# Kernel optimization log

Hardware: AMD Instinct MI355X
Metric: run time of the kernel (lower is better)

## Reference

```python
import jax, jax.numpy as jnp
import numpy as np


def _att(h, g, adj, a1, a2):
    # h: [B,N,D], g: [B,M,D], adj: [B,N,M] (int), a1/a2: [D,1]
    e1 = jnp.matmul(h, a1)                    # [B,N,1]
    e2 = jnp.matmul(g, a2).transpose(0, 2, 1)  # [B,1,M]
    e = jax.nn.leaky_relu(e1 + e2, negative_slope=0.2)  # [B,N,M]
    neg = jnp.asarray(-9.0e15, e.dtype)
    att = jnp.where(adj > 0, e, neg)
    att = jax.nn.softmax(att, axis=2)
    att = jnp.where(jnp.isnan(att), jnp.zeros_like(att), att)
    # degree renorm: adj[bs].sum(1).repeat(M,1).T == row degree broadcast over M
    deg = jnp.sum(adj, axis=2, keepdims=True).astype(e.dtype)  # [B,N,1]
    return jnp.matmul(att * deg, g)            # [B,N,D]


def setup_inputs() -> dict:
    key = jax.random.key(0)
    ks = jax.random.split(key, 13)
    B, N1, N2 = 64, 1024, 512
    F0, F1, D = 512, 384, 256
    return {
        "x0": jax.random.normal(ks[0], (B, N1, F0), jnp.float32),
        "x1": jax.random.normal(ks[1], (B, N2, F1), jnp.float32),
        "W0": jax.random.normal(ks[2], (F0, D), jnp.float32) * (1.414 / np.sqrt(F0)),
        "W1": jax.random.normal(ks[3], (F1, D), jnp.float32) * (1.414 / np.sqrt(F1)),
        "a1_0": jax.random.normal(ks[4], (D, 1), jnp.float32) * 0.1,
        "a2_0": jax.random.normal(ks[5], (D, 1), jnp.float32) * 0.1,
        "a1_1": jax.random.normal(ks[6], (D, 1), jnp.float32) * 0.1,
        "a2_1": jax.random.normal(ks[7], (D, 1), jnp.float32) * 0.1,
        "bias": jax.random.uniform(ks[8], (D,), jnp.float32, -1.0 / np.sqrt(D), 1.0 / np.sqrt(D)),
        "adj00": jax.random.randint(ks[9], (B, N1, N1), 0, 2, jnp.int32),
        "adj01": jax.random.randint(ks[10], (B, N1, N2), 0, 2, jnp.int32),
        "adj10": jax.random.randint(ks[11], (B, N2, N1), 0, 2, jnp.int32),
        "adj11": jax.random.randint(ks[12], (B, N2, N2), 0, 2, jnp.int32),
    }


def reference(x0, x1, W0, W1, a1_0, a2_0, a1_1, a2_1, bias,
              adj00, adj01, adj10, adj11):
    h0 = jnp.matmul(x0, W0)  # [B,N1,D]
    h1 = jnp.matmul(x1, W1)  # [B,N2,D]
    o00 = _att(h0, h0, adj00, a1_0, a2_0) + bias
    o01 = _att(h0, h1, adj01, a1_0, a2_0) + bias
    o10 = _att(h1, h0, adj10, a1_1, a2_1) + bias
    o11 = _att(h1, h1, adj11, a1_1, a2_1) + bias
    return (o00, o01, o10, o11)
```

## Files before the change

kernel.cpp:

```cpp
#include <hip/hip_runtime.h>

typedef __bf16 bf16x8 __attribute__((ext_vector_type(8)));
typedef float f32x4 __attribute__((ext_vector_type(4)));

static __device__ __forceinline__ ushort f2bf(float f) {
  uint u = __builtin_bit_cast(uint, f);
  u += 0x7fffu + ((u >> 16) & 1u);
  return (ushort)(u >> 16);
}
static __device__ __forceinline__ float bf2f(ushort h) {
  uint u = ((uint)h) << 16;
  return __builtin_bit_cast(float, u);
}

__global__ void detect9(const ushort* p0, const ushort* p1, const ushort* p2,
                        const ushort* p3, const ushort* p4, const ushort* p5,
                        const ushort* p6, const ushort* p7, const ushort* p8,
                        int* flags) {
  const ushort* ps[9] = {p0, p1, p2, p3, p4, p5, p6, p7, p8};
  const ushort* p = ps[blockIdx.x];
  int t = threadIdx.x;
  ushort u = p[2 * t];
  int e = (u >> 7) & 0xFF;
  int sane = (e >= 100 && e <= 150) ? 1 : 0;
  unsigned long long m = __ballot(sane);
  if (t == 0) flags[blockIdx.x] = (__popcll(m) >= 48) ? 0 : 1;
}

static __device__ __forceinline__ float ldf(const void* p, int is32, size_t i) {
  return is32 ? ((const float*)p)[i] : bf2f(((const ushort*)p)[i]);
}

__global__ void transw(const void* W, ushort* __restrict__ WT,
                       const int* __restrict__ flags, int fi, int F) {
  int is32 = flags[fi];
  int i = blockIdx.x * 256 + threadIdx.x;
  int k = i >> 8, d = i & 255;
  ushort v = is32 ? f2bf(((const float*)W)[i]) : ((const ushort*)W)[i];
  WT[(size_t)d * F + k] = v;
}

__global__ __launch_bounds__(256) void wa_k(const void* W, const void* a1, const void* a2,
                                            const void* a3, const int* __restrict__ flags,
                                            int fW, int f1, int f2, int f3,
                                            float* __restrict__ wa, int F) {
  __shared__ float al[3][256];
  int t = threadIdx.x;
  al[0][t] = ldf(a1, flags[f1], t);
  al[1][t] = ldf(a2, flags[f2], t);
  al[2][t] = ldf(a3, flags[f3], t);
  __syncthreads();
  int k = blockIdx.x * 256 + t;
  if (k < F) {
    int w32 = flags[fW];
    float s0 = 0.f, s1 = 0.f, s2 = 0.f;
    for (int d = 0; d < 256; d++) {
      float wv = ldf(W, w32, (size_t)k * 256 + d);
      s0 += wv * al[0][d]; s1 += wv * al[1][d]; s2 += wv * al[2][d];
    }
    wa[k] = s0; wa[F + k] = s1; wa[2 * F + k] = s2;
  }
}

__global__ __launch_bounds__(256) void evec_x(const void* __restrict__ x,
                                              const float* __restrict__ wa,
                                              const int* __restrict__ flags, int fi,
                                              float* __restrict__ o1, float* __restrict__ o2,
                                              float* __restrict__ o3, int F) {
  int x32 = flags[fi];
  int node = blockIdx.x * 4 + (threadIdx.x >> 6);
  int lane = threadIdx.x & 63;
  const float* wa1 = wa, *wa2 = wa + F, *wa3 = wa + 2 * F;
  float s1 = 0.f, s2 = 0.f, s3 = 0.f;
  size_t base = (size_t)node * F;
  for (int k = lane; k < F; k += 64) {
    float xv = ldf(x, x32, base + k);
    s1 += xv * wa1[k]; s2 += xv * wa2[k]; s3 += xv * wa3[k];
  }
  #pragma unroll
  for (int off = 1; off < 64; off <<= 1) {
    s1 += __shfl_xor(s1, off); s2 += __shfl_xor(s2, off); s3 += __shfl_xor(s3, off);
  }
  if (lane == 0) { o1[node] = s1; o2[node] = s2; o3[node] = s3; }
}

__global__ __launch_bounds__(256) void gemm_h(const void* __restrict__ x,
                                              const ushort* __restrict__ WT,
                                              ushort* __restrict__ hT,
                                              const int* __restrict__ flags, int fi,
                                              int N, int F) {
  int x32 = flags[fi];
  int ntiles = N >> 6;
  int b  = blockIdx.x / ntiles;
  int n0 = (blockIdx.x % ntiles) << 6;
  __shared__ ushort Al[64][72];
  __shared__ ushort Bl[256][72];
  int t = threadIdx.x, wave = t >> 6, lane = t & 63;
  f32x4 acc[4][4] = {};

  for (int k0 = 0; k0 < F; k0 += 64) {
    #pragma unroll
    for (int i = 0; i < 2; i++) {
      int r = (t >> 3) + i * 32, g = t & 7;
      if (!x32) {
        const ushort* xb = (const ushort*)x + (size_t)(b * N + n0 + r) * F + k0;
        ((uint4*)&Al[r][0])[g] = ((const uint4*)xb)[g];
      } else {
        const float* xf = (const float*)x + (size_t)(b * N + n0 + r) * F + k0;
        float4 fa = ((const float4*)xf)[2 * g];
        float4 fb = ((const float4*)xf)[2 * g + 1];
        union { ushort u[8]; uint4 q; } pk;
        pk.u[0] = f2bf(fa.x); pk.u[1] = f2bf(fa.y); pk.u[2] = f2bf(fa.z); pk.u[3] = f2bf(fa.w);
        pk.u[4] = f2bf(fb.x); pk.u[5] = f2bf(fb.y); pk.u[6] = f2bf(fb.z); pk.u[7] = f2bf(fb.w);
        ((uint4*)&Al[r][0])[g] = pk.q;
      }
    }
    #pragma unroll
    for (int i = 0; i < 8; i++) {
      int d = (t >> 3) + i * 32, g = t & 7;
      ((uint4*)&Bl[d][0])[g] = ((const uint4*)(WT + (size_t)d * F + k0))[g];
    }
    __syncthreads();
    #pragma unroll
    for (int kh = 0; kh < 2; kh++) {
      int kk = kh * 32 + ((lane >> 4) << 3);
      bf16x8 af[4], bfr[4];
      #pragma unroll
      for (int rf = 0; rf < 4; rf++) af[rf]  = *(const bf16x8*)&Al[rf * 16 + (lane & 15)][kk];
      #pragma unroll
      for (int cf = 0; cf < 4; cf++) bfr[cf] = *(const bf16x8*)&Bl[wave * 64 + cf * 16 + (lane & 15)][kk];
      #pragma unroll
      for (int rf = 0; rf < 4; rf++)
        #pragma unroll
        for (int cf = 0; cf < 4; cf++)
          acc[rf][cf] = __builtin_amdgcn_mfma_f32_16x16x32_bf16(af[rf], bfr[cf], acc[rf][cf], 0, 0, 0);
    }
    __syncthreads();
  }
  #pragma unroll
  for (int rf = 0; rf < 4; rf++) {
    int n = n0 + rf * 16 + ((lane >> 4) << 2);
    #pragma unroll
    for (int cf = 0; cf < 4; cf++) {
      int d = wave * 64 + cf * 16 + (lane & 15);
      ushort4 v;
      v.x = f2bf(acc[rf][cf][0]); v.y = f2bf(acc[rf][cf][1]);
      v.z = f2bf(acc[rf][cf][2]); v.w = f2bf(acc[rf][cf][3]);
      *(ushort4*)(hT + ((size_t)b * 256 + d) * N + n) = v;
    }
  }
}

__global__ __launch_bounds__(256) void att(const float* __restrict__ e1,
                                           const float* __restrict__ e2,
                                           const ushort* __restrict__ gT,
                                           const int* __restrict__ adj,
                                           const void* bias,
                                           const int* __restrict__ flags,
                                           void* __restrict__ outv, size_t ooff,
                                           int Nr, int M) {
  int b32 = flags[8];
  int o32 = flags[0] | flags[1] | flags[2] | flags[3] | flags[4] |
            flags[5] | flags[6] | flags[7] | flags[8];
  int ntiles = Nr >> 6;
  int b  = blockIdx.x / ntiles;
  int n0 = (blockIdx.x % ntiles) << 6;
  __shared__ ushort Wl[64][72];
  __shared__ ushort Gl[256][72];
  __shared__ float  e2l[1024];
  __shared__ float  e1l[64];
  __shared__ float  rscale[64];
  int t = threadIdx.x, wave = t >> 6, lane = t & 63;
  for (int i = t; i < M; i += 256) e2l[i] = e2[(size_t)b * M + i];
  if (t < 64) e1l[t] = e1[(size_t)b * Nr + n0 + t];
  __syncthreads();

  f32x4 acc[4][4] = {};
  float s_part = 0.f, deg_part = 0.f;
  int r = t >> 2, mseg = (t & 3) << 4;
  float e1v = e1l[r];
  const int* adjrow = adj + ((size_t)b * Nr + n0 + r) * M;

  for (int m0 = 0; m0 < M; m0 += 64) {
    #pragma unroll
    for (int i = 0; i < 8; i++) {
      int d = (t >> 3) + i * 32, g = t & 7;
      ((uint4*)&Gl[d][0])[g] = ((const uint4*)(gT + ((size_t)b * 256 + d) * M + m0))[g];
    }
    {
      const int* ap = adjrow + m0 + mseg;
      int4 q0 = ((const int4*)ap)[0], q1 = ((const int4*)ap)[1];
      int4 q2 = ((const int4*)ap)[2], q3 = ((const int4*)ap)[3];
      int av[16] = {q0.x,q0.y,q0.z,q0.w, q1.x,q1.y,q1.z,q1.w,
                    q2.x,q2.y,q2.z,q2.w, q3.x,q3.y,q3.z,q3.w};
      union { ushort u[16]; uint4 q[2]; } pk;
      #pragma unroll
      for (int j = 0; j < 16; j++) {
        float e = e1v + e2l[m0 + mseg + j];
        e = e > 0.f ? e : 0.2f * e;
        e = fminf(e, 60.f);
        float w = (av[j] > 0) ? __expf(e) : 0.f;
        ushort wb = f2bf(w);
        s_part += bf2f(wb);
        deg_part += (float)av[j];
        pk.u[j] = wb;
      }
      *(uint4*)&Wl[r][mseg]     = pk.q[0];
      *(uint4*)&Wl[r][mseg + 8] = pk.q[1];
    }
    __syncthreads();
    #pragma unroll
    for (int kh = 0; kh < 2; kh++) {
      int kk = kh * 32 + ((lane >> 4) << 3);
      bf16x8 af[4], bfr[4];
      #pragma unroll
      for (int rf = 0; rf < 4; rf++) af[rf]  = *(const bf16x8*)&Wl[rf * 16 + (lane & 15)][kk];
      #pragma unroll
      for (int cf = 0; cf < 4; cf++) bfr[cf] = *(const bf16x8*)&Gl[wave * 64 + cf * 16 + (lane & 15)][kk];
      #pragma unroll
      for (int rf = 0; rf < 4; rf++)
        #pragma unroll
        for (int cf = 0; cf < 4; cf++)
          acc[rf][cf] = __builtin_amdgcn_mfma_f32_16x16x32_bf16(af[rf], bfr[cf], acc[rf][cf], 0, 0, 0);
    }
    __syncthreads();
  }

  s_part   += __shfl_xor(s_part, 1);   s_part   += __shfl_xor(s_part, 2);
  deg_part += __shfl_xor(deg_part, 1); deg_part += __shfl_xor(deg_part, 2);
  if ((t & 3) == 0) {
    float sc = (s_part > 0.f) ? deg_part / s_part : 0.f;
    if (!(sc > -1e38f && sc < 1e38f)) sc = 0.f;
    rscale[r] = sc;
  }
  __syncthreads();

  #pragma unroll
  for (int rf = 0; rf < 4; rf++) {
    int nbase = rf * 16 + ((lane >> 4) << 2);
    #pragma unroll
    for (int cf = 0; cf < 4; cf++) {
      int d = wave * 64 + cf * 16 + (lane & 15);
      float bi = ldf(bias, b32, d);
      #pragma unroll
      for (int j = 0; j < 4; j++) {
        int nl = nbase + j;
        float v = acc[rf][cf][j] * rscale[nl] + bi;
        size_t idx = ooff + ((size_t)(b * Nr + n0 + nl)) * 256 + d;
        if (o32) ((float*)outv)[idx] = v;
        else     ((ushort*)outv)[idx] = f2bf(v);
      }
    }
  }
}

extern "C" void kernel_launch(void* const* d_in, const int* in_sizes, int n_in,
                              void* d_out, int out_size, void* d_ws, size_t ws_size,
                              hipStream_t stream) {
  (void)in_sizes; (void)n_in; (void)out_size; (void)ws_size;
  const void* x0   = d_in[0];
  const void* x1   = d_in[1];
  const void* W0   = d_in[2];
  const void* W1   = d_in[3];
  const void* a1_0 = d_in[4];
  const void* a2_0 = d_in[5];
  const void* a1_1 = d_in[6];
  const void* a2_1 = d_in[7];
  const void* bias = d_in[8];
  const int* adj00 = (const int*)d_in[9];
  const int* adj01 = (const int*)d_in[10];
  const int* adj10 = (const int*)d_in[11];
  const int* adj11 = (const int*)d_in[12];

  const int B = 64, N1 = 1024, N2 = 512, F0 = 512, F1 = 384;
  int*    flags = (int*)d_ws;
  ushort* base = (ushort*)((char*)d_ws + 64);
  ushort* hT0 = base;
  ushort* hT1 = hT0 + (size_t)B * 256 * N1;
  ushort* WT0 = hT1 + (size_t)B * 256 * N2;
  ushort* WT1 = WT0 + (size_t)256 * F0;
  float* e1_0 = (float*)(WT1 + (size_t)256 * F1);
  float* e2a  = e1_0 + (size_t)B * N1;
  float* e2c  = e2a + (size_t)B * N1;
  float* e1_1 = e2c + (size_t)B * N1;
  float* e2b  = e1_1 + (size_t)B * N2;
  float* e2d  = e2b + (size_t)B * N2;
  float* wa0  = e2d + (size_t)B * N2;
  float* wa1  = wa0 + 3 * F0;

  detect9<<<9, 64, 0, stream>>>((const ushort*)x0, (const ushort*)x1,
                                (const ushort*)W0, (const ushort*)W1,
                                (const ushort*)a1_0, (const ushort*)a2_0,
                                (const ushort*)a1_1, (const ushort*)a2_1,
                                (const ushort*)bias, flags);

  transw<<<F0, 256, 0, stream>>>(W0, WT0, flags, 2, F0);
  transw<<<F1, 256, 0, stream>>>(W1, WT1, flags, 3, F1);
  wa_k<<<(F0 + 255) / 256, 256, 0, stream>>>(W0, a1_0, a2_0, a2_1, flags, 2, 4, 5, 7, wa0, F0);
  wa_k<<<(F1 + 255) / 256, 256, 0, stream>>>(W1, a1_1, a2_0, a2_1, flags, 3, 6, 5, 7, wa1, F1);
  gemm_h<<<B * (N1 / 64), 256, 0, stream>>>(x0, WT0, hT0, flags, 0, N1, F0);
  gemm_h<<<B * (N2 / 64), 256, 0, stream>>>(x1, WT1, hT1, flags, 1, N2, F1);
  evec_x<<<B * N1 / 4, 256, 0, stream>>>(x0, wa0, flags, 0, e1_0, e2a, e2c, F0);
  evec_x<<<B * N2 / 4, 256, 0, stream>>>(x1, wa1, flags, 1, e1_1, e2b, e2d, F1);

  const size_t o00 = 0;
  const size_t o01 = (size_t)B * N1 * 256;
  const size_t o10 = o01 + (size_t)B * N1 * 256;
  const size_t o11 = o10 + (size_t)B * N2 * 256;
  att<<<B * (N1 / 64), 256, 0, stream>>>(e1_0, e2a, hT0, adj00, bias, flags, d_out, o00, N1, N1);
  att<<<B * (N1 / 64), 256, 0, stream>>>(e1_0, e2b, hT1, adj01, bias, flags, d_out, o01, N1, N2);
  att<<<B * (N2 / 64), 256, 0, stream>>>(e1_1, e2c, hT0, adj10, bias, flags, d_out, o10, N2, N1);
  att<<<B * (N2 / 64), 256, 0, stream>>>(e1_1, e2d, hT1, adj11, bias, flags, d_out, o11, N2, N2);
}
```

Before: 1.071 ms.

## Stage B/G tiles via direct global-to-LDS loads with XOR swizzle, prefetch next tiles

Both the projection GEMM and the attention kernel now load the 256x64 weight/feature tile straight into LDS with global_load_lds, storing it unpadded with an XOR swizzle on the 16-byte chunk index. The reads apply the same swizzle to avoid bank conflicts. The x rows and adjacency values for the next k/m tile are register-prefetched one iteration ahead so their global latency overlaps the current MFMA work. This removes the VGPR round trip for the large tile and hides some load latency, at the cost of more live registers and a tighter correctness dependency on the swizzle and LDS-load layout matching.

```diff
diff --git a/kernel.cpp b/kernel.cpp
--- a/kernel.cpp
+++ b/kernel.cpp
@@ -2,6 +2,9 @@
 
 typedef __bf16 bf16x8 __attribute__((ext_vector_type(8)));
 typedef float f32x4 __attribute__((ext_vector_type(4)));
+
+#define GPTR(p) ((const __attribute__((address_space(1))) void*)(p))
+#define LPTR(p) ((__attribute__((address_space(3))) void*)(p))
 
 static __device__ __forceinline__ ushort f2bf(float f) {
   uint u = __builtin_bit_cast(uint, f);
@@ -84,6 +87,39 @@
   if (lane == 0) { o1[node] = s1; o2[node] = s2; o3[node] = s3; }
 }
 
+static __device__ __forceinline__ void stage_tile(const ushort* __restrict__ src,
+                                                  int rowstride,
+                                                  ushort* __restrict__ dst,
+                                                  int wave, int lane) {
+  int rsub = lane >> 3;
+  int gsw = ((lane & 7) ^ rsub) << 3;
+  #pragma unroll
+  for (int i = 0; i < 8; i++) {
+    int dbase = i * 32 + wave * 8;
+    __builtin_amdgcn_global_load_lds(
+        GPTR(src + (size_t)(dbase + rsub) * rowstride + gsw),
+        LPTR(dst + dbase * 64), 16, 0, 0);
+  }
+}
+
+static __device__ __forceinline__ void load_x4(uint4* dst, const void* x, int x32,
+                                               size_t rowbase, int F, int k0,
+                                               int r0, int g8) {
+  if (x32) {
+    #pragma unroll
+    for (int i = 0; i < 2; i++) {
+      const uint4* xf = (const uint4*)((const float*)x + (rowbase + (size_t)(r0 + i * 32)) * F + k0);
+      dst[2 * i] = xf[2 * g8]; dst[2 * i + 1] = xf[2 * g8 + 1];
+    }
+  } else {
+    #pragma unroll
+    for (int i = 0; i < 2; i++) {
+      const uint4* xb = (const uint4*)((const ushort*)x + (rowbase + (size_t)(r0 + i * 32)) * F + k0);
+      dst[i] = xb[g8];
+    }
+  }
+}
+
 __global__ __launch_bounds__(256) void gemm_h(const void* __restrict__ x,
                                               const ushort* __restrict__ WT,
                                               ushort* __restrict__ hT,
@@ -94,41 +130,48 @@
   int b  = blockIdx.x / ntiles;
   int n0 = (blockIdx.x % ntiles) << 6;
   __shared__ ushort Al[64][72];
-  __shared__ ushort Bl[256][72];
+  __shared__ ushort Bl[256 * 64];
   int t = threadIdx.x, wave = t >> 6, lane = t & 63;
+  int r0 = t >> 3, g8 = t & 7;
+  size_t rowbase = (size_t)(b * N + n0);
   f32x4 acc[4][4] = {};
 
-  for (int k0 = 0; k0 < F; k0 += 64) {
-    #pragma unroll
-    for (int i = 0; i < 2; i++) {
-      int r = (t >> 3) + i * 32, g = t & 7;
-      if (!x32) {
-        const ushort* xb = (const ushort*)x + (size_t)(b * N + n0 + r) * F + k0;
-        ((uint4*)&Al[r][0])[g] = ((const uint4*)xb)[g];
-      } else {
-        const float* xf = (const float*)x + (size_t)(b * N + n0 + r) * F + k0;
-        float4 fa = ((const float4*)xf)[2 * g];
-        float4 fb = ((const float4*)xf)[2 * g + 1];
+  const int nk = F >> 6;
+  uint4 xr[4], xn[4];
+  load_x4(xr, x, x32, rowbase, F, 0, r0, g8);
+
+  for (int kt = 0; kt < nk; kt++) {
+    int k0 = kt << 6;
+    int has_next = (kt + 1 < nk);
+    stage_tile(WT + k0, F, Bl, wave, lane);
+    if (has_next) load_x4(xn, x, x32, rowbase, F, k0 + 64, r0, g8);
+    if (x32) {
+      #pragma unroll
+      for (int i = 0; i < 2; i++) {
+        union { uint4 q[2]; float f[8]; } fa;
+        fa.q[0] = xr[2 * i]; fa.q[1] = xr[2 * i + 1];
         union { ushort u[8]; uint4 q; } pk;
-        pk.u[0] = f2bf(fa.x); pk.u[1] = f2bf(fa.y); pk.u[2] = f2bf(fa.z); pk.u[3] = f2bf(fa.w);
-        pk.u[4] = f2bf(fb.x); pk.u[5] = f2bf(fb.y); pk.u[6] = f2bf(fb.z); pk.u[7] = f2bf(fb.w);
-        ((uint4*)&Al[r][0])[g] = pk.q;
-      }
-    }
-    #pragma unroll
-    for (int i = 0; i < 8; i++) {
-      int d = (t >> 3) + i * 32, g = t & 7;
-      ((uint4*)&Bl[d][0])[g] = ((const uint4*)(WT + (size_t)d * F + k0))[g];
+        #pragma unroll
+        for (int j = 0; j < 8; j++) pk.u[j] = f2bf(fa.f[j]);
+        ((uint4*)&Al[r0 + i * 32][0])[g8] = pk.q;
+      }
+    } else {
+      #pragma unroll
+      for (int i = 0; i < 2; i++) ((uint4*)&Al[r0 + i * 32][0])[g8] = xr[i];
     }
     __syncthreads();
     #pragma unroll
     for (int kh = 0; kh < 2; kh++) {
       int kk = kh * 32 + ((lane >> 4) << 3);
+      int sw = (lane & 7) << 3;
       bf16x8 af[4], bfr[4];
       #pragma unroll
       for (int rf = 0; rf < 4; rf++) af[rf]  = *(const bf16x8*)&Al[rf * 16 + (lane & 15)][kk];
       #pragma unroll
-      for (int cf = 0; cf < 4; cf++) bfr[cf] = *(const bf16x8*)&Bl[wave * 64 + cf * 16 + (lane & 15)][kk];
+      for (int cf = 0; cf < 4; cf++) {
+        int d = wave * 64 + cf * 16 + (lane & 15);
+        bfr[cf] = *(const bf16x8*)(Bl + d * 64 + (kk ^ sw));
+      }
       #pragma unroll
       for (int rf = 0; rf < 4; rf++)
         #pragma unroll
@@ -136,6 +179,10 @@
           acc[rf][cf] = __builtin_amdgcn_mfma_f32_16x16x32_bf16(af[rf], bfr[cf], acc[rf][cf], 0, 0, 0);
     }
     __syncthreads();
+    if (has_next) {
+      #pragma unroll
+      for (int j = 0; j < 4; j++) xr[j] = xn[j];
+    }
   }
   #pragma unroll
   for (int rf = 0; rf < 4; rf++) {
@@ -166,7 +213,7 @@
   int b  = blockIdx.x / ntiles;
   int n0 = (blockIdx.x % ntiles) << 6;
   __shared__ ushort Wl[64][72];
-  __shared__ ushort Gl[256][72];
+  __shared__ ushort Gl[256 * 64];
   __shared__ float  e2l[1024];
   __shared__ float  e1l[64];
   __shared__ float  rscale[64];
@@ -180,19 +227,27 @@
   int r = t >> 2, mseg = (t & 3) << 4;
   float e1v = e1l[r];
   const int* adjrow = adj + ((size_t)b * Nr + n0 + r) * M;
-
-  for (int m0 = 0; m0 < M; m0 += 64) {
-    #pragma unroll
-    for (int i = 0; i < 8; i++) {
-      int d = (t >> 3) + i * 32, g = t & 7;
-      ((uint4*)&Gl[d][0])[g] = ((const uint4*)(gT + ((size_t)b * 256 + d) * M + m0))[g];
+  const ushort* gbase = gT + (size_t)b * 256 * M;
+
+  int4 qc0 = ((const int4*)(adjrow + mseg))[0];
+  int4 qc1 = ((const int4*)(adjrow + mseg))[1];
+  int4 qc2 = ((const int4*)(adjrow + mseg))[2];
+  int4 qc3 = ((const int4*)(adjrow + mseg))[3];
+
+  const int nm = M >> 6;
+  for (int mt = 0; mt < nm; mt++) {
+    int m0 = mt << 6;
+    int has_next = (mt + 1 < nm);
+    stage_tile(gbase + m0, M, Gl, wave, lane);
+    int4 qn0, qn1, qn2, qn3;
+    if (has_next) {
+      const int* apn = adjrow + m0 + 64 + mseg;
+      qn0 = ((const int4*)apn)[0]; qn1 = ((const int4*)apn)[1];
+      qn2 = ((const int4*)apn)[2]; qn3 = ((const int4*)apn)[3];
     }
     {
-      const int* ap = adjrow + m0 + mseg;
-      int4 q0 = ((const int4*)ap)[0], q1 = ((const int4*)ap)[1];
-      int4 q2 = ((const int4*)ap)[2], q3 = ((const int4*)ap)[3];
-      int av[16] = {q0.x,q0.y,q0.z,q0.w, q1.x,q1.y,q1.z,q1.w,
-                    q2.x,q2.y,q2.z,q2.w, q3.x,q3.y,q3.z,q3.w};
+      int av[16] = {qc0.x,qc0.y,qc0.z,qc0.w, qc1.x,qc1.y,qc1.z,qc1.w,
+                    qc2.x,qc2.y,qc2.z,qc2.w, qc3.x,qc3.y,qc3.z,qc3.w};
       union { ushort u[16]; uint4 q[2]; } pk;
       #pragma unroll
       for (int j = 0; j < 16; j++) {
@@ -212,11 +267,15 @@
     #pragma unroll
     for (int kh = 0; kh < 2; kh++) {
       int kk = kh * 32 + ((lane >> 4) << 3);
+      int sw = (lane & 7) << 3;
       bf16x8 af[4], bfr[4];
       #pragma unroll
       for (int rf = 0; rf < 4; rf++) af[rf]  = *(const bf16x8*)&Wl[rf * 16 + (lane & 15)][kk];
       #pragma unroll
-      for (int cf = 0; cf < 4; cf++) bfr[cf] = *(const bf16x8*)&Gl[wave * 64 + cf * 16 + (lane & 15)][kk];
+      for (int cf = 0; cf < 4; cf++) {
+        int d = wave * 64 + cf * 16 + (lane & 15);
+        bfr[cf] = *(const bf16x8*)(Gl + d * 64 + (kk ^ sw));
+      }
       #pragma unroll
       for (int rf = 0; rf < 4; rf++)
         #pragma unroll
@@ -224,6 +283,7 @@
           acc[rf][cf] = __builtin_amdgcn_mfma_f32_16x16x32_bf16(af[rf], bfr[cf], acc[rf][cf], 0, 0, 0);
     }
     __syncthreads();
+    if (has_next) { qc0 = qn0; qc1 = qn1; qc2 = qn2; qc3 = qn3; }
   }
 
   s_part   += __shfl_xor(s_part, 1);   s_part   += __shfl_xor(s_part, 2);
```

Measured after the change: 1.162 ms. +8.5%, slower.
